# Kernel tuning notes

Measured on AMD Instinct MI355X. Metric: run time of the kernel, lower is better.

## Reference

```python
import jax, jax.numpy as jnp
import numpy as np

WS = 8          # window size (8x8)
HEADS = 8
DIM_HEAD = 28
SCALE = DIM_HEAD ** -0.5


def _window_partition(t, ws=WS):
    # [b, H, W, c] -> [b, n_windows, ws*ws, c]
    b, H, W, c = t.shape
    t = t.reshape(b, H // ws, ws, W // ws, ws, c)
    t = t.transpose(0, 1, 3, 2, 4, 5)
    return t.reshape(b, (H // ws) * (W // ws), ws * ws, c)


def _window_reverse(t, H, W, ws=WS):
    # [b, n_windows, ws*ws, c] -> [b, H, W, c]
    b = t.shape[0]
    c = t.shape[-1]
    t = t.reshape(b, H // ws, W // ws, ws, ws, c)
    t = t.transpose(0, 1, 3, 2, 4, 5)
    return t.reshape(b, H, W, c)


def _heads_split(t, nh):
    # [b, n, mm, (nh*d)] -> [b, n, nh, mm, d]
    b, n, mm, cd = t.shape
    return t.reshape(b, n, mm, nh, cd // nh).transpose(0, 1, 3, 2, 4)


def setup_inputs() -> dict:
    key = jax.random.key(0)
    ks = jax.random.split(key, 6)
    b, H, W, c = 128, 32, 32, 224
    inner = DIM_HEAD * HEADS  # 224
    return {
        "x": jax.random.normal(ks[0], (b, H, W, c), jnp.float32),
        "Wq": jax.random.normal(ks[1], (c, inner), jnp.float32) * (c ** -0.5),
        "Wkv": jax.random.normal(ks[2], (c, 2 * inner), jnp.float32) * (c ** -0.5),
        "Wout": jax.random.normal(ks[3], (inner, c), jnp.float32) * (inner ** -0.5),
        "bout": jnp.zeros((c,), jnp.float32),
        "pos_emb1": jax.random.normal(ks[4], (1, 1, HEADS // 2, WS * WS, WS * WS), jnp.float32),
        "pos_emb2": jax.random.normal(ks[5], (1, 1, HEADS // 2, 16, 16), jnp.float32),
    }


def reference(x, Wq, Wkv, Wout, bout, pos_emb1, pos_emb2):
    b, H, W, c = x.shape
    nh = HEADS // 2  # heads per branch

    q = x @ Wq                       # [b,H,W,224]
    kv = x @ Wkv
    k, v = jnp.split(kv, 2, axis=-1)

    half = c // 2
    q1, q2 = q[..., :half], q[..., half:]
    k1, k2 = k[..., :half], k[..., half:]
    v1, v2 = v[..., :half], v[..., half:]

    # ----- local branch: attention within each 8x8 window -----
    q1 = _heads_split(_window_partition(q1), nh) * SCALE  # [b,n,nh,64,d]
    k1 = _heads_split(_window_partition(k1), nh)
    v1 = _heads_split(_window_partition(v1), nh)
    sim1 = jnp.einsum('bnhid,bnhjd->bnhij', q1, k1) + pos_emb1
    attn1 = jax.nn.softmax(sim1, axis=-1)
    out1 = jnp.einsum('bnhij,bnhjd->bnhid', attn1, v1)    # [b,n,nh,64,d]
    bN = out1.shape[1]
    out1 = out1.transpose(0, 1, 3, 2, 4).reshape(b, bN, WS * WS, half)

    # ----- global branch: attention across windows (same in-window position) -----
    def part_global(t):
        t = _window_partition(t)                 # [b,n,mm,half]
        t = t.transpose(0, 2, 1, 3)              # [b,mm,n,half]
        return _heads_split(t, nh)               # [b,mm,nh,n,d]
    q2 = part_global(q2) * SCALE
    k2 = part_global(k2)
    v2 = part_global(v2)
    sim2 = jnp.einsum('bnhid,bnhjd->bnhij', q2, k2) + pos_emb2
    attn2 = jax.nn.softmax(sim2, axis=-1)
    out2 = jnp.einsum('bnhij,bnhjd->bnhid', attn2, v2)    # [b,mm,nh,n,d]
    out2 = out2.transpose(0, 1, 3, 2, 4).reshape(b, WS * WS, bN, half)
    out2 = out2.transpose(0, 2, 1, 3)                     # [b,n,mm,half]

    out = jnp.concatenate([out1, out2], axis=-1)          # [b,n,mm,c]
    out = out @ Wout + bout
    return _window_reverse(out, H, W)
```

## Files before the change

kernel.cpp:

```cpp
#include <hip/hip_runtime.h>
#include <stdint.h>

typedef short s8v __attribute__((ext_vector_type(8)));
typedef float f4v __attribute__((ext_vector_type(4)));
typedef unsigned short u16;

#define MFMA16(a, b, c) __builtin_amdgcn_mfma_f32_16x16x32_bf16(a, b, c, 0, 0, 0)
#define SCALE 0.1889822365046136f

__device__ __forceinline__ u16 f2bf(float f) {
  union { float f; uint32_t u; } v;
  v.f = f;
  uint32_t u = v.u;
  u += 0x7fffu + ((u >> 16) & 1u);
  return (u16)(u >> 16);
}

__device__ __forceinline__ void gld_lds16(const void* g, void* l) {
  __builtin_amdgcn_global_load_lds(
      (const __attribute__((address_space(1))) void*)g,
      (__attribute__((address_space(3))) void*)l, 16, 0, 0);
}

__global__ void prep_kernel(const float4* __restrict__ x4,
                            const float* __restrict__ Wq,
                            const float* __restrict__ Wkv,
                            const float* __restrict__ Wout,
                            u16* __restrict__ xb,
                            u16* __restrict__ wqkvt,
                            u16* __restrict__ woutt) {
  const int gsz = gridDim.x * blockDim.x;
  const int gt = blockIdx.x * blockDim.x + threadIdx.x;
  for (int i = gt; i < 7340032; i += gsz) {
    float4 v = x4[i];
    ushort4 o;
    o.x = f2bf(v.x); o.y = f2bf(v.y); o.z = f2bf(v.z); o.w = f2bf(v.w);
    ((ushort4*)xb)[i] = o;
  }
  for (int i = gt; i < 768 * 224; i += gsz) {
    const int n = i / 224, k = i - n * 224;
    float v = 0.f;
    if (n < 224) v = Wq[k * 224 + n];
    else if (n < 672) v = Wkv[k * 448 + (n - 224)];
    wqkvt[i] = f2bf(v);
  }
  for (int i = gt; i < 256 * 224; i += gsz) {
    const int n = i / 224, k = i - n * 224;
    const float v = (n < 224) ? Wout[k * 224 + n] : 0.f;
    woutt[i] = f2bf(v);
  }
}

template <int OUT_F32, int NTILES>
__global__ __launch_bounds__(256) void gemm_af(const u16* __restrict__ Ap,
                                               const u16* __restrict__ Bt,
                                               void* __restrict__ Cp,
                                               const float* __restrict__ bias,
                                               int Nvalid, int ldc) {
  extern __shared__ u16 smem[];
  u16* As  = smem;
  u16* Bs0 = smem + 28672;
  u16* Bs1 = smem + 32768;
  const int tid = threadIdx.x;
  const int wave = tid >> 6, lane = tid & 63;
  const int c16 = lane & 15, g = lane >> 4;
  const int m0 = blockIdx.x * 128;
  const int wm = wave & 1, wn = wave >> 1;

  const int fbw = wave * 1024 + lane * 16;
  const int brow0 = fbw >> 6, bcol0 = (fbw & 63) >> 1;

#define STAGE_B(ntile, ktile, bufp)                                            \
  do {                                                                         \
    char* bb = (char*)((bufp) ? Bs1 : Bs0) + wave * 1024;                      \
    const u16* src =                                                           \
        Bt + (size_t)((ntile) * 128 + brow0) * 224 + (ktile) * 32 + bcol0;     \
    gld_lds16(src, bb);                                                        \
    gld_lds16(src + (size_t)64 * 224, bb + 4096);                              \
  } while (0)

  STAGE_B(0, 0, 0);
  if (NTILES * 7 > 1) STAGE_B(0, 1, 1);

  for (int rnd = 0; rnd < 14; ++rnd) {
    const int fb = rnd * 4096 + fbw;
    const int row = fb / 448;
    const int off = fb - row * 448;
    gld_lds16(Ap + (size_t)(m0 + row) * 224 + (off >> 1),
              (char*)As + rnd * 4096 + wave * 1024);
  }
  __syncthreads();

  for (int nt = 0; nt < NTILES; ++nt) {
    f4v acc[4][4] = {};
    for (int kt = 0; kt < 7; ++kt) {
      const int t = nt * 7 + kt;
      const u16* Bs = (t & 1) ? Bs1 : Bs0;
      s8v af[4], bf[4];
      for (int tt = 0; tt < 4; ++tt)
        af[tt] = *(const s8v*)&As[(wm * 64 + tt * 16 + c16) * 224 + kt * 32 + g * 8];
      for (int tt = 0; tt < 4; ++tt)
        bf[tt] = *(const s8v*)&Bs[(wn * 64 + tt * 16 + c16) * 32 + g * 8];
      for (int i = 0; i < 4; ++i)
        for (int j = 0; j < 4; ++j)
          acc[i][j] = MFMA16(af[i], bf[j], acc[i][j]);
      __syncthreads();
      const int ns = t + 2;
      if (ns < NTILES * 7) {
        const int nnt = ns / 7;
        STAGE_B(nnt, ns - nnt * 7, t & 1);
      }
    }
    const int n0 = nt * 128;
    for (int i = 0; i < 4; ++i) {
      const int rowb = m0 + wm * 64 + i * 16 + g * 4;
      for (int j = 0; j < 4; ++j) {
        const int col = n0 + wn * 64 + j * 16 + c16;
        if (col < Nvalid) {
          if (OUT_F32) {
            const float bz = bias[col];
            for (int r = 0; r < 4; ++r)
              ((float*)Cp)[(size_t)(rowb + r) * ldc + col] = acc[i][j][r] + bz;
          } else {
            for (int r = 0; r < 4; ++r)
              ((u16*)Cp)[(size_t)(rowb + r) * ldc + col] = f2bf(acc[i][j][r]);
          }
        }
      }
    }
  }
#undef STAGE_B
}

__global__ __launch_bounds__(256, 3) void attn_fused(
    const u16* __restrict__ xb, const u16* __restrict__ Wt,
    const float* __restrict__ pos1, const float* __restrict__ pos2,
    u16* __restrict__ attn) {
  extern __shared__ u16 sm[];
  u16* As0 = sm;
  u16* As1 = sm + 2048;
  u16* Bs0 = sm + 4096;
  u16* Bs1 = sm + 14848;
  const int blk0 = blockIdx.x;
  const int local = (blk0 < 2048) ? 1 : 0;
  const int blk = local ? blk0 : blk0 - 2048;
  const int tid = threadIdx.x;
  const int wave = tid >> 6, lane = tid & 63;
  const int c16 = lane & 15, g = lane >> 4;
  const int b = blk >> 4, sub = blk & 15;

  int base_s = 0, ig = 0;
  if (local) {
    base_s = (b * 32 + (sub >> 2) * 8) * 32 + (sub & 3) * 8;
  } else {
    ig = sub;
  }

  int s_a;
  {
    const int arow = tid >> 2;
    if (local) {
      s_a = base_s + (arow >> 3) * 32 + (arow & 7);
    } else {
      const int w2 = arow >> 4, j = arow & 15;
      const int ii = ig * 4 + w2;
      const int y = ii >> 3, x = ii & 7;
      s_a = (b * 32 + (j >> 2) * 8 + y) * 32 + (j & 3) * 8 + x;
    }
  }
  const int a_off = (tid & 3) * 8;

#define STAGE_A(ktile, buf)                                                   \
  gld_lds16(xb + (size_t)s_a * 224 + (ktile) * 32 + a_off,                    \
            (char*)(buf) + tid * 16)

  const int qoff = local ? 0 : 112;
#define STAGE_W(ktile, buf)                                                   \
  do {                                                                        \
    for (int mm = 0; mm < 6; ++mm) {                                          \
      const int ch = mm * 256 + tid;                                          \
      if (ch < 1344) {                                                        \
        const int brow = ch >> 2, bc = (ch & 3) * 8;                          \
        const int n = qoff + brow + ((brow >= 112) ? 112 : 0) +               \
                      ((brow >= 224) ? 112 : 0);                              \
        gld_lds16(Wt + (size_t)n * 224 + (ktile) * 32 + bc,                   \
                  (char*)(buf) + ch * 16);                                    \
      }                                                                       \
    }                                                                         \
  } while (0)

  STAGE_A(0, As0);
  STAGE_W(0, Bs0);
  STAGE_A(1, As1);
  STAGE_W(1, Bs1);
  __syncthreads();

  f4v acc[6][4] = {};
  for (int kt = 0; kt < 7; ++kt) {
    const u16* Bs = (kt & 1) ? Bs1 : Bs0;
    const u16* Asb = (kt & 1) ? As1 : As0;
    s8v af[4];
#pragma unroll
    for (int st = 0; st < 4; ++st)
      af[st] = *(const s8v*)&Asb[(st * 16 + c16) * 32 + g * 8];
#pragma unroll
    for (int j = 0; j < 6; ++j) {
      const int tile = j * 4 + wave;
      if (tile < 21) {
        const s8v bf = *(const s8v*)&Bs[(tile * 16 + c16) * 32 + g * 8];
#pragma unroll
        for (int st = 0; st < 4; ++st)
          acc[j][st] = MFMA16(af[st], bf, acc[j][st]);
      }
    }
    __syncthreads();
    if (kt + 2 < 7) {
      STAGE_A(kt + 2, (kt & 1) ? As1 : As0);
      STAGE_W(kt + 2, (kt & 1) ? Bs1 : Bs0);
    }
  }

  u16* qs  = sm;
  u16* ks  = sm + 8192;
  u16* pm  = sm;
  u16* vtL = sm + 18432;
  u16* vtG = sm + 16384;
  u16* p2  = sm + 24608;

#pragma unroll
  for (int j = 0; j < 6; ++j) {
    const int tile = j * 4 + wave;
    if (tile < 21) {
      const int seg = (tile >= 14) ? 2 : ((tile >= 7) ? 1 : 0);
      const int nn = tile * 16 + c16 - seg * 112;
      const int h = ((nn >= 28) ? 1 : 0) + ((nn >= 56) ? 1 : 0) + ((nn >= 84) ? 1 : 0);
      const int d = nn - h * 28;
#pragma unroll
      for (int st = 0; st < 4; ++st) {
        if (seg == 2) {
          ushort4 o;
          o.x = f2bf(acc[j][st][0]); o.y = f2bf(acc[j][st][1]);
          o.z = f2bf(acc[j][st][2]); o.w = f2bf(acc[j][st][3]);
          if (local)
            *(ushort4*)&vtL[(h * 28 + d) * 72 + st * 16 + g * 4] = o;
          else
            *(ushort4*)&vtG[st * 2056 + (h * 32 + d) * 16 + g * 4] = o;
        } else {
          u16* dst = seg ? ks : qs;
#pragma unroll
          for (int r = 0; r < 4; ++r) {
            const u16 v = f2bf(acc[j][st][r]);
            if (local)
              dst[(h * 64 + st * 16 + g * 4 + r) * 32 + d] = v;
            else
              dst[((st * 4 + h) * 16 + g * 4 + r) * 32 + d] = v;
          }
        }
      }
    }
  }
  {
    const ushort4 z = {0, 0, 0, 0};
    *(ushort4*)(qs + tid * 32 + 28) = z;
    *(ushort4*)(ks + tid * 32 + 28) = z;
    if (!local) {
      const int w2 = tid >> 6, hq = (tid >> 4) & 3;
      const int dd = 28 + ((tid >> 2) & 3), j4 = tid & 3;
      *(ushort4*)(vtG + w2 * 2056 + (hq * 32 + dd) * 16 + j4 * 4) = z;
    }
  }
  __syncthreads();

  const f4v fz = {0.f, 0.f, 0.f, 0.f};
  if (local) {
    const int h = wave;
    s8v af2[4], bf2[4];
    for (int t = 0; t < 4; ++t)
      af2[t] = *(const s8v*)&qs[(h * 64 + t * 16 + c16) * 32 + g * 8];
    for (int t = 0; t < 4; ++t)
      bf2[t] = *(const s8v*)&ks[(h * 64 + t * 16 + c16) * 32 + g * 8];
    f4v sc[4][4];
    for (int i = 0; i < 4; ++i)
      for (int j = 0; j < 4; ++j)
        sc[i][j] = MFMA16(af2[i], bf2[j], fz);
    float lrow[4][4];
    const float* ph = pos1 + h * 4096;
    for (int i = 0; i < 4; ++i) {
      for (int r = 0; r < 4; ++r) {
        const int irow = i * 16 + g * 4 + r;
        float mx = -1e30f;
        for (int j = 0; j < 4; ++j) {
          const float v = sc[i][j][r] * SCALE + ph[irow * 64 + j * 16 + c16];
          sc[i][j][r] = v;
          mx = fmaxf(mx, v);
        }
        for (int dd = 1; dd < 16; dd <<= 1) mx = fmaxf(mx, __shfl_xor(mx, dd, 64));
        float sum = 0.f;
        for (int j = 0; j < 4; ++j) {
          const float e = __expf(sc[i][j][r] - mx);
          sc[i][j][r] = e;
          sum += e;
        }
        for (int dd = 1; dd < 16; dd <<= 1) sum += __shfl_xor(sum, dd, 64);
        lrow[i][r] = sum;
      }
    }
    __syncthreads();
    for (int i = 0; i < 4; ++i)
      for (int r = 0; r < 4; ++r) {
        const int irow = i * 16 + g * 4 + r;
        for (int j = 0; j < 4; ++j)
          pm[(h * 64 + irow) * 72 + j * 16 + c16] = f2bf(sc[i][j][r]);
      }
    f4v o[4][2] = {};
    for (int kk = 0; kk < 2; ++kk) {
      s8v ap[4], bv[2];
      for (int t = 0; t < 4; ++t)
        ap[t] = *(const s8v*)&pm[(h * 64 + t * 16 + c16) * 72 + kk * 32 + g * 8];
      for (int t = 0; t < 2; ++t)
        bv[t] = *(const s8v*)&vtL[(h * 28 + t * 16 + c16) * 72 + kk * 32 + g * 8];
      for (int i = 0; i < 4; ++i)
        for (int j = 0; j < 2; ++j)
          o[i][j] = MFMA16(ap[i], bv[j], o[i][j]);
    }
    for (int i = 0; i < 4; ++i)
      for (int r = 0; r < 4; ++r) {
        const int irow = i * 16 + g * 4 + r;
        const int s = base_s + (irow >> 3) * 32 + (irow & 7);
        const float inv = 1.f / lrow[i][r];
        for (int j = 0; j < 2; ++j) {
          const int d = j * 16 + c16;
          if (d < 28)
            attn[(size_t)s * 224 + h * 28 + d] = f2bf(o[i][j][r] * inv);
        }
      }
  } else {
    const int w = wave;
    const int i = ig * 4 + w;
    const int y = i >> 3, x = i & 7;
    const int w4 = w * 4;
    for (int h = 0; h < 4; ++h) {
      const s8v aq = *(const s8v*)&qs[((w4 + h) * 16 + c16) * 32 + g * 8];
      const s8v bk = *(const s8v*)&ks[((w4 + h) * 16 + c16) * 32 + g * 8];
      const f4v s = MFMA16(aq, bk, fz);
      const float* ph = pos2 + h * 256;
      float l[4];
      for (int r = 0; r < 4; ++r) {
        const float v = s[r] * SCALE + ph[(g * 4 + r) * 16 + c16];
        float mx = v;
        for (int dd = 1; dd < 16; dd <<= 1) mx = fmaxf(mx, __shfl_xor(mx, dd, 64));
        const float e = __expf(v - mx);
        float sum = e;
        for (int dd = 1; dd < 16; dd <<= 1) sum += __shfl_xor(sum, dd, 64);
        l[r] = sum;
        p2[(w * 16 + g * 4 + r) * 32 + c16] = f2bf(e);
        p2[(w * 16 + g * 4 + r) * 32 + c16 + 16] = 0;
      }
      const s8v ap = *(const s8v*)&p2[(w * 16 + c16) * 32 + g * 8];
      f4v o[2];
      for (int nt = 0; nt < 2; ++nt) {
        s8v bv = {0, 0, 0, 0, 0, 0, 0, 0};
        if (g < 2)
          bv = *(const s8v*)&vtG[w * 2056 + (h * 32 + nt * 16 + c16) * 16 + g * 8];
        o[nt] = MFMA16(ap, bv, fz);
      }
      for (int nt = 0; nt < 2; ++nt)
        for (int r = 0; r < 4; ++r) {
          const int d = nt * 16 + c16;
          if (d < 28) {
            const int wi = g * 4 + r;
            const int sw = (b * 32 + (wi >> 2) * 8 + y) * 32 + (wi & 3) * 8 + x;
            attn[(size_t)sw * 224 + 112 + h * 28 + d] = f2bf(o[nt][r] / l[r]);
          }
        }
    }
  }
#undef STAGE_W
#undef STAGE_A
}

extern "C" void kernel_launch(void* const* d_in, const int* in_sizes, int n_in,
                              void* d_out, int out_size, void* d_ws, size_t ws_size,
                              hipStream_t stream) {
  const float* x    = (const float*)d_in[0];
  const float* Wq   = (const float*)d_in[1];
  const float* Wkv  = (const float*)d_in[2];
  const float* Wout = (const float*)d_in[3];
  const float* bout = (const float*)d_in[4];
  const float* pos1 = (const float*)d_in[5];
  const float* pos2 = (const float*)d_in[6];
  char* ws = (char*)d_ws;
  u16* xb    = (u16*)ws;
  u16* attn  = (u16*)(ws + 58720256);
  u16* wqkvt = (u16*)(ws + 117440512);
  u16* woutt = (u16*)(ws + 117784576);

  prep_kernel<<<dim3(1024), 256, 0, stream>>>(
      (const float4*)x, Wq, Wkv, Wout, xb, wqkvt, woutt);

  attn_fused<<<dim3(4096), 256, 53568, stream>>>(xb, wqkvt, pos1, pos2, attn);

  gemm_af<1, 2><<<dim3(1024), 256, 73728, stream>>>(attn, woutt, d_out, bout, 224, 224);
}
```

Measured before the change: 349.1 us.

## Pre-swizzle QKV weights into MFMA fragment order and load directly to registers

The prep kernel now writes the QKV weight matrix in a per-16-column-tile, per-k-tile fragment layout so each lane's 8-element B operand is contiguous. The fused attention kernel drops the LDS staging of weights and instead loads B fragments straight from global memory into registers, prefetching the next k-tile one iteration ahead. This removes large LDS weight traffic and its staging instructions, shrinking shared memory use, at the cost of more registers and relying on L2/cache hits for the repeated weight reads across blocks.

Result: slower. 533.8 us (+52.9%).

```diff
diff --git a/kernel.cpp b/kernel.cpp
--- a/kernel.cpp
+++ b/kernel.cpp
@@ -27,7 +27,7 @@
                             const float* __restrict__ Wkv,
                             const float* __restrict__ Wout,
                             u16* __restrict__ xb,
-                            u16* __restrict__ wqkvt,
+                            u16* __restrict__ w2,
                             u16* __restrict__ woutt) {
   const int gsz = gridDim.x * blockDim.x;
   const int gt = blockIdx.x * blockDim.x + threadIdx.x;
@@ -37,12 +37,18 @@
     o.x = f2bf(v.x); o.y = f2bf(v.y); o.z = f2bf(v.z); o.w = f2bf(v.w);
     ((ushort4*)xb)[i] = o;
   }
-  for (int i = gt; i < 768 * 224; i += gsz) {
-    const int n = i / 224, k = i - n * 224;
+  for (int i = gt; i < 172032; i += gsz) {
+    const int e = i & 7;
+    const int l = (i >> 3) & 63;
+    const int wtkt = i >> 9;
+    const int wt = wtkt / 7;
+    const int kt = wtkt - wt * 7;
+    const int n = wt * 16 + (l & 15);
+    const int kk = kt * 32 + (l >> 4) * 8 + e;
     float v = 0.f;
-    if (n < 224) v = Wq[k * 224 + n];
-    else if (n < 672) v = Wkv[k * 448 + (n - 224)];
-    wqkvt[i] = f2bf(v);
+    if (n < 224) v = Wq[kk * 224 + n];
+    else if (n < 672) v = Wkv[kk * 448 + (n - 224)];
+    w2[i] = f2bf(v);
   }
   for (int i = gt; i < 256 * 224; i += gsz) {
     const int n = i / 224, k = i - n * 224;
@@ -133,14 +139,12 @@
 }
 
 __global__ __launch_bounds__(256, 3) void attn_fused(
-    const u16* __restrict__ xb, const u16* __restrict__ Wt,
+    const u16* __restrict__ xb, const u16* __restrict__ W2,
     const float* __restrict__ pos1, const float* __restrict__ pos2,
     u16* __restrict__ attn) {
   extern __shared__ u16 sm[];
   u16* As0 = sm;
   u16* As1 = sm + 2048;
-  u16* Bs0 = sm + 4096;
-  u16* Bs1 = sm + 14848;
   const int blk0 = blockIdx.x;
   const int local = (blk0 < 2048) ? 1 : 0;
   const int blk = local ? blk0 : blk0 - 2048;
@@ -162,8 +166,8 @@
     if (local) {
       s_a = base_s + (arow >> 3) * 32 + (arow & 7);
     } else {
-      const int w2 = arow >> 4, j = arow & 15;
-      const int ii = ig * 4 + w2;
+      const int w2i = arow >> 4, j = arow & 15;
+      const int ii = ig * 4 + w2i;
       const int y = ii >> 3, x = ii & 7;
       s_a = (b * 32 + (j >> 2) * 8 + y) * 32 + (j & 3) * 8 + x;
     }
@@ -174,30 +178,43 @@
   gld_lds16(xb + (size_t)s_a * 224 + (ktile) * 32 + a_off,                    \
             (char*)(buf) + tid * 16)
 
-  const int qoff = local ? 0 : 112;
-#define STAGE_W(ktile, buf)                                                   \
-  do {                                                                        \
-    for (int mm = 0; mm < 6; ++mm) {                                          \
-      const int ch = mm * 256 + tid;                                          \
-      if (ch < 1344) {                                                        \
-        const int brow = ch >> 2, bc = (ch & 3) * 8;                          \
-        const int n = qoff + brow + ((brow >= 112) ? 112 : 0) +               \
-                      ((brow >= 224) ? 112 : 0);                              \
-        gld_lds16(Wt + (size_t)n * 224 + (ktile) * 32 + bc,                   \
-                  (char*)(buf) + ch * 16);                                    \
-      }                                                                       \
-    }                                                                         \
-  } while (0)
-
   STAGE_A(0, As0);
-  STAGE_W(0, Bs0);
   STAGE_A(1, As1);
-  STAGE_W(1, Bs1);
+
+  const u16* wp[6];
+#pragma unroll
+  for (int j = 0; j < 6; ++j) {
+    const int t = j * 4 + wave;
+    const int seg = (t >= 14) ? 2 : ((t >= 7) ? 1 : 0);
+    const int wtile = t + 7 * seg + (local ? 0 : 7);
+    wp[j] = W2 + ((size_t)(wtile * 7) << 9) + lane * 8;
+  }
+
+#pragma unroll
+  for (int j = 0; j < 6; ++j) {
+    const int t = j * 4 + wave;
+    const int seg = (t >= 14) ? 2 : ((t >= 7) ? 1 : 0);
+    const int wtile = t + 7 * seg + (local ? 0 : 7);
+    wp[j] = W2 + (size_t)(wtile * 7) * 512 + lane * 8;
+  }
+
+  s8v wf[6];
+#pragma unroll
+  for (int j = 0; j < 6; ++j)
+    if (j * 4 + wave < 21) wf[j] = *(const s8v*)(wp[j]);
+
   __syncthreads();
 
   f4v acc[6][4] = {};
+#pragma unroll
   for (int kt = 0; kt < 7; ++kt) {
-    const u16* Bs = (kt & 1) ? Bs1 : Bs0;
+    s8v wfn[6];
+    if (kt < 6) {
+#pragma unroll
+      for (int j = 0; j < 6; ++j)
+        if (j * 4 + wave < 21)
+          wfn[j] = *(const s8v*)(wp[j] + (kt + 1) * 512);
+    }
     const u16* Asb = (kt & 1) ? As1 : As0;
     s8v af[4];
 #pragma unroll
@@ -205,18 +222,17 @@
       af[st] = *(const s8v*)&Asb[(st * 16 + c16) * 32 + g * 8];
 #pragma unroll
     for (int j = 0; j < 6; ++j) {
-      const int tile = j * 4 + wave;
-      if (tile < 21) {
-        const s8v bf = *(const s8v*)&Bs[(tile * 16 + c16) * 32 + g * 8];
+      if (j * 4 + wave < 21) {
 #pragma unroll
         for (int st = 0; st < 4; ++st)
-          acc[j][st] = MFMA16(af[st], bf, acc[j][st]);
+          acc[j][st] = MFMA16(af[st], wf[j], acc[j][st]);
       }
     }
     __syncthreads();
-    if (kt + 2 < 7) {
-      STAGE_A(kt + 2, (kt & 1) ? As1 : As0);
-      STAGE_W(kt + 2, (kt & 1) ? Bs1 : Bs0);
+    if (kt + 2 < 7) STAGE_A(kt + 2, (kt & 1) ? As1 : As0);
+    if (kt < 6) {
+#pragma unroll
+      for (int j = 0; j < 6; ++j) wf[j] = wfn[j];
     }
   }
 
@@ -264,9 +280,9 @@
     *(ushort4*)(qs + tid * 32 + 28) = z;
     *(ushort4*)(ks + tid * 32 + 28) = z;
     if (!local) {
-      const int w2 = tid >> 6, hq = (tid >> 4) & 3;
+      const int w2i = tid >> 6, hq = (tid >> 4) & 3;
       const int dd = 28 + ((tid >> 2) & 3), j4 = tid & 3;
-      *(ushort4*)(vtG + w2 * 2056 + (hq * 32 + dd) * 16 + j4 * 4) = z;
+      *(ushort4*)(vtG + w2i * 2056 + (hq * 32 + dd) * 16 + j4 * 4) = z;
     }
   }
   __syncthreads();
@@ -375,7 +391,6 @@
         }
     }
   }
-#undef STAGE_W
 #undef STAGE_A
 }
 
@@ -392,13 +407,13 @@
   char* ws = (char*)d_ws;
   u16* xb    = (u16*)ws;
   u16* attn  = (u16*)(ws + 58720256);
-  u16* wqkvt = (u16*)(ws + 117440512);
+  u16* w2    = (u16*)(ws + 117440512);
   u16* woutt = (u16*)(ws + 117784576);
 
   prep_kernel<<<dim3(1024), 256, 0, stream>>>(
-      (const float4*)x, Wq, Wkv, Wout, xb, wqkvt, woutt);
-
-  attn_fused<<<dim3(4096), 256, 53568, stream>>>(xb, wqkvt, pos1, pos2, attn);
+      (const float4*)x, Wq, Wkv, Wout, xb, w2, woutt);
+
+  attn_fused<<<dim3(4096), 256, 53312, stream>>>(xb, w2, pos1, pos2, attn);
 
   gemm_af<1, 2><<<dim3(1024), 256, 73728, stream>>>(attn, woutt, d_out, bout, 224, 224);
 }
```
